# Optimization experiments

Measured on AMD Instinct MI355X. Metric: run time of the kernel, lower is better.

Reference implementation:

```python
import jax, jax.numpy as jnp
import numpy as np
import math

B, IN, H = 4096, 1024, 1024

def setup_inputs() -> dict:
    key = jax.random.key(0)
    ks = jax.random.split(key, 20)
    stdv = 1.0 / math.sqrt(H)
    def U(k, shape):
        return jax.random.uniform(k, shape, jnp.float32, -stdv, stdv)
    inp = {
        'input_': jax.random.normal(ks[0], (B, IN), jnp.float32),
        'prev_h': jax.random.normal(ks[1], (B, H), jnp.float32),
        'prev_c': jax.random.normal(ks[2], (B, H), jnp.float32),
    }
    names = ['ii', 'hi', 'if_', 'hf', 'ig', 'hg', 'io', 'ho']
    for n, kw, kb in zip(names, ks[3:11], ks[11:19]):
        in_dim = IN if n[0] == 'i' else H
        inp['W_' + n] = U(kw, (H, in_dim))  # torch Linear weight is (out, in)
        inp['b_' + n] = U(kb, (H,))
    return inp

def reference(input_, prev_h, prev_c,
              W_ii, b_ii, W_hi, b_hi, W_if_, b_if_, W_hf, b_hf,
              W_ig, b_ig, W_hg, b_hg, W_io, b_io, W_ho, b_ho):
    # Fuse the 8 small GEMMs into 2 batched GEMMs over stacked gate weights.
    Wx = jnp.concatenate([W_ii, W_if_, W_ig, W_io], axis=0)   # (4H, IN)
    Wh = jnp.concatenate([W_hi, W_hf, W_hg, W_ho], axis=0)    # (4H, H)
    bx = jnp.concatenate([b_ii, b_if_, b_ig, b_io], axis=0)   # (4H,)
    bh = jnp.concatenate([b_hi, b_hf, b_hg, b_ho], axis=0)
    gates = input_ @ Wx.T + prev_h @ Wh.T + bx + bh           # (B, 4H)
    i, f, g, o = jnp.split(gates, 4, axis=-1)
    i = jax.nn.sigmoid(i)
    f = jax.nn.sigmoid(f)
    g = jnp.tanh(g)
    o = jax.nn.sigmoid(o)
    c = f * prev_c + i * g
    h = o * jnp.tanh(c)
    return (h, c)
```

## Files before the change

### kernel.cpp

```cpp
#include <hip/hip_runtime.h>
#include <hip/hip_bf16.h>
#include <stdint.h>


typedef __attribute__((ext_vector_type(8))) short bf16x8;
typedef __attribute__((ext_vector_type(4))) float f32x4;
typedef __attribute__((ext_vector_type(8))) unsigned short u16x8;

__device__ __forceinline__ unsigned short f2bf(float f) {
  union { float f; uint32_t u; } v; v.f = f;
  uint32_t u = v.u;
  u += 0x7FFFu + ((u >> 16) & 1);
  return (unsigned short)(u >> 16);
}
__device__ __forceinline__ float fast_sigmoid(float x) { return 1.f / (1.f + __expf(-x)); }
__device__ __forceinline__ float fast_tanh(float x) { return 1.f - 2.f / (1.f + __expf(2.f * x)); }

__global__ __launch_bounds__(256) void pack_kernel(
    const float* __restrict__ x, const float* __restrict__ hprev,
    const float* __restrict__ W_ii, const float* __restrict__ W_if,
    const float* __restrict__ W_ig, const float* __restrict__ W_io,
    const float* __restrict__ W_hi, const float* __restrict__ W_hf,
    const float* __restrict__ W_hg, const float* __restrict__ W_ho,
    unsigned short* __restrict__ Ap, unsigned short* __restrict__ Wp) {
  const int bid = blockIdx.x;
  const int k = threadIdx.x << 3;
  const float* src;
  unsigned short* dst;
  if (bid < 4096) {
    const int b = bid;
    src = (k < 1024) ? (x + (size_t)b * 1024 + k) : (hprev + (size_t)b * 1024 + (k - 1024));
    dst = Ap + (size_t)b * 2048 + k;
  } else {
    const int rp = bid - 4096;
    const int g = (rp >> 4) & 3;
    const int u = ((rp >> 6) << 4) | (rp & 15);
    const float* wx = (g == 0) ? W_ii : (g == 1) ? W_if : (g == 2) ? W_ig : W_io;
    const float* wh = (g == 0) ? W_hi : (g == 1) ? W_hf : (g == 2) ? W_hg : W_ho;
    src = (k < 1024) ? (wx + (size_t)u * 1024 + k) : (wh + (size_t)u * 1024 + (k - 1024));
    dst = Wp + (size_t)rp * 2048 + k;
  }
  float4 v0 = *(const float4*)src;
  float4 v1 = *(const float4*)(src + 4);
  u16x8 o;
  o[0] = f2bf(v0.x); o[1] = f2bf(v0.y); o[2] = f2bf(v0.z); o[3] = f2bf(v0.w);
  o[4] = f2bf(v1.x); o[5] = f2bf(v1.y); o[6] = f2bf(v1.z); o[7] = f2bf(v1.w);
  *(u16x8*)dst = o;
}


#define GL16(g, l)                                                                   \
  __builtin_amdgcn_global_load_lds(                                                  \
      (const __attribute__((address_space(1))) unsigned int*)(g),                    \
      (__attribute__((address_space(3))) unsigned int*)(l), 16, 0, 0)

#define STAGE_A(BUF, H, KT)                                                          \
  { GL16(pA0 + (size_t)(H) * 524288 + (size_t)(KT) * 128,                            \
         lds + (BUF) * 32768 + (H) * 16384 + wvoff);                                 \
    GL16(pA1 + (size_t)(H) * 524288 + (size_t)(KT) * 128,                            \
         lds + (BUF) * 32768 + (H) * 16384 + 8192 + wvoff); }
#define STAGE_B(BUF, H, KT)                                                          \
  { GL16(pB0 + (size_t)(H) * 524288 + (size_t)(KT) * 128,                            \
         lds + 65536 + (BUF) * 32768 + (H) * 16384 + wvoff);                         \
    GL16(pB1 + (size_t)(H) * 524288 + (size_t)(KT) * 128,                            \
         lds + 65536 + (BUF) * 32768 + (H) * 16384 + 8192 + wvoff); }

#define DS_A(BUF, QQ)                                                                \
  { const char* Ab_ = lds + (BUF) * 32768 + tbA + (QQ) * 4096;                       \
    a00 = *(const bf16x8*)(Ab_ + off0);        a01 = *(const bf16x8*)(Ab_ + off1);   \
    a10 = *(const bf16x8*)(Ab_ + 2048 + off0); a11 = *(const bf16x8*)(Ab_ + 2048 + off1); }

#define DS_B(BUF)                                                                    \
  { const char* Bb_ = lds + 65536 + (BUF) * 32768 + tbB;                             \
    _Pragma("unroll")                                                                \
    for (int ni = 0; ni < 4; ++ni) {                                                 \
      breg[ni][0] = *(const bf16x8*)(Bb_ + ni * 2048 + off0);                        \
      breg[ni][1] = *(const bf16x8*)(Bb_ + ni * 2048 + off1);                        \
    } }

#define MFMA_CLUSTER(QQ)                                                             \
  { __builtin_amdgcn_s_setprio(1);                                                   \
    _Pragma("unroll")                                                                \
    for (int ni = 0; ni < 4; ++ni) {                                                 \
      acc[2*(QQ)][ni]   = __builtin_amdgcn_mfma_f32_16x16x32_bf16(a00, breg[ni][0], acc[2*(QQ)][ni], 0,0,0);   \
      acc[2*(QQ)][ni]   = __builtin_amdgcn_mfma_f32_16x16x32_bf16(a01, breg[ni][1], acc[2*(QQ)][ni], 0,0,0);   \
      acc[2*(QQ)+1][ni] = __builtin_amdgcn_mfma_f32_16x16x32_bf16(a10, breg[ni][0], acc[2*(QQ)+1][ni], 0,0,0); \
      acc[2*(QQ)+1][ni] = __builtin_amdgcn_mfma_f32_16x16x32_bf16(a11, breg[ni][1], acc[2*(QQ)+1][ni], 0,0,0); \
    }                                                                                \
    __builtin_amdgcn_s_setprio(0); }

#define BAR()      __builtin_amdgcn_s_barrier()
#define LGKM0()    asm volatile("s_waitcnt lgkmcnt(0)" ::: "memory")
#define LGKM8()    asm volatile("s_waitcnt lgkmcnt(8)" ::: "memory")
#define VMC4()     asm volatile("s_waitcnt vmcnt(4)" ::: "memory")

__global__ __launch_bounds__(512, 2) void lstm_gemm_kernel(
    const unsigned short* __restrict__ Ap, const unsigned short* __restrict__ Wp,
    const float* __restrict__ b_ii, const float* __restrict__ b_hi,
    const float* __restrict__ b_if, const float* __restrict__ b_hf,
    const float* __restrict__ b_ig, const float* __restrict__ b_hg,
    const float* __restrict__ b_io, const float* __restrict__ b_ho,
    const float* __restrict__ prev_c,
    float* __restrict__ out_h, float* __restrict__ out_c) {
  __shared__ char lds[131072];

  const int tid  = threadIdx.x;
  const int lane = tid & 63;
  const int wv   = tid >> 6;
  const int wm   = wv >> 2;
  const int wn   = wv & 3;

  const int bid = blockIdx.x;
  const int sid = (bid & 7) * 32 + (bid >> 3);
  const int bx  = sid & 15;
  const int by  = sid >> 4;

  const int r0  = tid >> 3;
  const int r1  = (tid + 512) >> 3;
  const int kb0 = (((tid & 7) ^ ((r0 >> 1) & 7)) << 4);
  const int kb1 = (((tid & 7) ^ ((r1 >> 1) & 7)) << 4);
  const char* ApC = (const char*)Ap;
  const char* BpC = (const char*)Wp;
  const char* pA0 = ApC + (size_t)(bx * 256 + r0) * 4096 + kb0;
  const char* pA1 = ApC + (size_t)(bx * 256 + r1) * 4096 + kb1;
  const char* pB0 = BpC + (size_t)(by * 256 + r0) * 4096 + kb0;
  const char* pB1 = BpC + (size_t)(by * 256 + r1) * 4096 + kb1;
  const int wvoff = wv * 1024;

  const int qe   = (lane >> 4) ^ ((lane >> 1) & 7);
  const int off0 = qe << 4;
  const int off1 = (qe ^ 4) << 4;
  const int tbA = (wm * 128 + (lane & 15)) * 128;
  const int tbB = (wn * 64 + (lane & 15)) * 128;

  f32x4 acc[8][4];
#pragma unroll
  for (int mi = 0; mi < 8; ++mi)
#pragma unroll
    for (int ni = 0; ni < 4; ++ni) acc[mi][ni] = (f32x4){0.f, 0.f, 0.f, 0.f};

  bf16x8 breg[4][2];
  bf16x8 a00, a01, a10, a11;

  STAGE_B(0, 0, 0); STAGE_B(0, 1, 0);
  STAGE_A(0, 0, 0); STAGE_A(0, 1, 0);
  STAGE_B(1, 0, 1); STAGE_B(1, 1, 1);
  VMC4();
  BAR();

  for (int i = 0; i < 16; ++i) {
    const int T  = i << 1;
    const int k1 = (T + 1) & 31;
    const int k2 = (T + 2) & 31;
    const int k3 = (T + 3) & 31;

    DS_B(0); DS_A(0, 0);
    STAGE_A(1, 0, k1);
    LGKM8();
    BAR(); LGKM0();
    MFMA_CLUSTER(0);
    BAR();
    DS_A(0, 1);
    STAGE_A(1, 1, k1);
    BAR(); LGKM0();
    MFMA_CLUSTER(1);
    BAR();
    DS_A(0, 2);
    STAGE_B(0, 0, k2);
    BAR(); LGKM0();
    MFMA_CLUSTER(2);
    BAR();
    DS_A(0, 3);
    STAGE_B(0, 1, k2);
    VMC4();
    BAR(); LGKM0();
    MFMA_CLUSTER(3);
    BAR();
    DS_B(1); DS_A(1, 0);
    STAGE_A(0, 0, k2);
    LGKM8();
    BAR(); LGKM0();
    MFMA_CLUSTER(0);
    BAR();
    DS_A(1, 1);
    STAGE_A(0, 1, k2);
    BAR(); LGKM0();
    MFMA_CLUSTER(1);
    BAR();
    DS_A(1, 2);
    STAGE_B(1, 0, k3);
    BAR(); LGKM0();
    MFMA_CLUSTER(2);
    BAR();
    DS_A(1, 3);
    STAGE_B(1, 1, k3);
    VMC4();
    BAR(); LGKM0();
    MFMA_CLUSTER(3);
    BAR();
  }

  const int u = ((by * 4 + wn) << 4) + (lane & 15);
  const float bsum0 = b_ii[u] + b_hi[u];
  const float bsum1 = b_if[u] + b_hf[u];
  const float bsum2 = b_ig[u] + b_hg[u];
  const float bsum3 = b_io[u] + b_ho[u];
  const int row0 = bx * 256 + wm * 128 + ((lane >> 4) << 2);

#pragma unroll
  for (int mi = 0; mi < 8; ++mi) {
#pragma unroll
    for (int rr = 0; rr < 4; ++rr) {
      const int row = row0 + mi * 16 + rr;
      const float gi = fast_sigmoid(acc[mi][0][rr] + bsum0);
      const float gf = fast_sigmoid(acc[mi][1][rr] + bsum1);
      const float gg = fast_tanh   (acc[mi][2][rr] + bsum2);
      const float go = fast_sigmoid(acc[mi][3][rr] + bsum3);
      const float cp = prev_c[(size_t)row * 1024 + u];
      const float c  = gf * cp + gi * gg;
      const float hh = go * fast_tanh(c);
      out_h[(size_t)row * 1024 + u] = hh;
      out_c[(size_t)row * 1024 + u] = c;
    }
  }
}


extern "C" void kernel_launch(void* const* d_in, const int* in_sizes, int n_in,
                              void* d_out, int out_size, void* d_ws, size_t ws_size,
                              hipStream_t stream) {
  const float* input_ = (const float*)d_in[0];
  const float* prev_h = (const float*)d_in[1];
  const float* prev_c = (const float*)d_in[2];
  const float* W_ii = (const float*)d_in[3];  const float* b_ii = (const float*)d_in[4];
  const float* W_hi = (const float*)d_in[5];  const float* b_hi = (const float*)d_in[6];
  const float* W_if = (const float*)d_in[7];  const float* b_if = (const float*)d_in[8];
  const float* W_hf = (const float*)d_in[9];  const float* b_hf = (const float*)d_in[10];
  const float* W_ig = (const float*)d_in[11]; const float* b_ig = (const float*)d_in[12];
  const float* W_hg = (const float*)d_in[13]; const float* b_hg = (const float*)d_in[14];
  const float* W_io = (const float*)d_in[15]; const float* b_io = (const float*)d_in[16];
  const float* W_ho = (const float*)d_in[17]; const float* b_ho = (const float*)d_in[18];

  unsigned short* Ap = (unsigned short*)d_ws;
  unsigned short* Wp = Ap + (size_t)4096 * 2048;

  pack_kernel<<<8192, 256, 0, stream>>>(input_, prev_h,
                                        W_ii, W_if, W_ig, W_io,
                                        W_hi, W_hf, W_hg, W_ho, Ap, Wp);

  float* out_h = (float*)d_out;
  float* out_c = out_h + (size_t)4096 * 1024;
  lstm_gemm_kernel<<<256, 512, 0, stream>>>(Ap, Wp,
                                            b_ii, b_hi, b_if, b_hf,
                                            b_ig, b_hg, b_io, b_ho,
                                            prev_c, out_h, out_c);
}
```

Before: 211.6 us.

## Double-buffer LDS fragment registers to overlap ds_reads with MFMA clusters

Splits the A and B register fragments into two ping-pong sets so the LDS reads for the next quarter-tile are issued before the MFMA cluster that consumes the current set. The explicit lgkmcnt waits are removed, which leaves the compiler to insert them. The aim is to hide LDS read latency behind matrix math instead of stalling before each cluster. In exchange it raises VGPR pressure under the 512-thread, 2-block launch bound, and the prefetch of the next B buffer happens later relative to its global staging, so correctness depends on the barrier placement.

```diff
diff --git a/kernel.cpp b/kernel.cpp
--- a/kernel.cpp
+++ b/kernel.cpp
@@ -65,33 +65,31 @@
     GL16(pB1 + (size_t)(H) * 524288 + (size_t)(KT) * 128,                            \
          lds + 65536 + (BUF) * 32768 + (H) * 16384 + 8192 + wvoff); }
 
-#define DS_A(BUF, QQ)                                                                \
+#define DS_A_INTO(A0f, A1f, A2f, A3f, BUF, QQ)                                       \
   { const char* Ab_ = lds + (BUF) * 32768 + tbA + (QQ) * 4096;                       \
-    a00 = *(const bf16x8*)(Ab_ + off0);        a01 = *(const bf16x8*)(Ab_ + off1);   \
-    a10 = *(const bf16x8*)(Ab_ + 2048 + off0); a11 = *(const bf16x8*)(Ab_ + 2048 + off1); }
-
-#define DS_B(BUF)                                                                    \
+    A0f = *(const bf16x8*)(Ab_ + off0);        A1f = *(const bf16x8*)(Ab_ + off1);   \
+    A2f = *(const bf16x8*)(Ab_ + 2048 + off0); A3f = *(const bf16x8*)(Ab_ + 2048 + off1); }
+
+#define DS_B_INTO(BR, BUF)                                                           \
   { const char* Bb_ = lds + 65536 + (BUF) * 32768 + tbB;                             \
     _Pragma("unroll")                                                                \
     for (int ni = 0; ni < 4; ++ni) {                                                 \
-      breg[ni][0] = *(const bf16x8*)(Bb_ + ni * 2048 + off0);                        \
-      breg[ni][1] = *(const bf16x8*)(Bb_ + ni * 2048 + off1);                        \
+      BR[ni][0] = *(const bf16x8*)(Bb_ + ni * 2048 + off0);                          \
+      BR[ni][1] = *(const bf16x8*)(Bb_ + ni * 2048 + off1);                          \
     } }
 
-#define MFMA_CLUSTER(QQ)                                                             \
+#define MFMA_C(QQ, A0f, A1f, A2f, A3f, BR)                                           \
   { __builtin_amdgcn_s_setprio(1);                                                   \
     _Pragma("unroll")                                                                \
     for (int ni = 0; ni < 4; ++ni) {                                                 \
-      acc[2*(QQ)][ni]   = __builtin_amdgcn_mfma_f32_16x16x32_bf16(a00, breg[ni][0], acc[2*(QQ)][ni], 0,0,0);   \
-      acc[2*(QQ)][ni]   = __builtin_amdgcn_mfma_f32_16x16x32_bf16(a01, breg[ni][1], acc[2*(QQ)][ni], 0,0,0);   \
-      acc[2*(QQ)+1][ni] = __builtin_amdgcn_mfma_f32_16x16x32_bf16(a10, breg[ni][0], acc[2*(QQ)+1][ni], 0,0,0); \
-      acc[2*(QQ)+1][ni] = __builtin_amdgcn_mfma_f32_16x16x32_bf16(a11, breg[ni][1], acc[2*(QQ)+1][ni], 0,0,0); \
+      acc[2*(QQ)][ni]   = __builtin_amdgcn_mfma_f32_16x16x32_bf16(A0f, BR[ni][0], acc[2*(QQ)][ni], 0,0,0);   \
+      acc[2*(QQ)][ni]   = __builtin_amdgcn_mfma_f32_16x16x32_bf16(A1f, BR[ni][1], acc[2*(QQ)][ni], 0,0,0);   \
+      acc[2*(QQ)+1][ni] = __builtin_amdgcn_mfma_f32_16x16x32_bf16(A2f, BR[ni][0], acc[2*(QQ)+1][ni], 0,0,0); \
+      acc[2*(QQ)+1][ni] = __builtin_amdgcn_mfma_f32_16x16x32_bf16(A3f, BR[ni][1], acc[2*(QQ)+1][ni], 0,0,0); \
     }                                                                                \
     __builtin_amdgcn_s_setprio(0); }
 
 #define BAR()      __builtin_amdgcn_s_barrier()
-#define LGKM0()    asm volatile("s_waitcnt lgkmcnt(0)" ::: "memory")
-#define LGKM8()    asm volatile("s_waitcnt lgkmcnt(8)" ::: "memory")
 #define VMC4()     asm volatile("s_waitcnt vmcnt(4)" ::: "memory")
 
 __global__ __launch_bounds__(512, 2) void lstm_gemm_kernel(
@@ -139,14 +137,16 @@
 #pragma unroll
     for (int ni = 0; ni < 4; ++ni) acc[mi][ni] = (f32x4){0.f, 0.f, 0.f, 0.f};
 
-  bf16x8 breg[4][2];
-  bf16x8 a00, a01, a10, a11;
+  bf16x8 bA[4][2], bB[4][2];
+  bf16x8 aX0, aX1, aX2, aX3, aY0, aY1, aY2, aY3;
 
   STAGE_B(0, 0, 0); STAGE_B(0, 1, 0);
   STAGE_A(0, 0, 0); STAGE_A(0, 1, 0);
   STAGE_B(1, 0, 1); STAGE_B(1, 1, 1);
   VMC4();
   BAR();
+  DS_B_INTO(bA, 0);
+  DS_A_INTO(aX0, aX1, aX2, aX3, 0, 0);
 
   for (int i = 0; i < 16; ++i) {
     const int T  = i << 1;
@@ -154,49 +154,49 @@
     const int k2 = (T + 2) & 31;
     const int k3 = (T + 3) & 31;
 
-    DS_B(0); DS_A(0, 0);
     STAGE_A(1, 0, k1);
-    LGKM8();
-    BAR(); LGKM0();
-    MFMA_CLUSTER(0);
-    BAR();
-    DS_A(0, 1);
+    BAR();
+    DS_A_INTO(aY0, aY1, aY2, aY3, 0, 1);
+    MFMA_C(0, aX0, aX1, aX2, aX3, bA);
+    BAR();
     STAGE_A(1, 1, k1);
-    BAR(); LGKM0();
-    MFMA_CLUSTER(1);
-    BAR();
-    DS_A(0, 2);
+    BAR();
+    DS_A_INTO(aX0, aX1, aX2, aX3, 0, 2);
+    MFMA_C(1, aY0, aY1, aY2, aY3, bA);
+    BAR();
     STAGE_B(0, 0, k2);
-    BAR(); LGKM0();
-    MFMA_CLUSTER(2);
-    BAR();
-    DS_A(0, 3);
+    BAR();
+    DS_A_INTO(aY0, aY1, aY2, aY3, 0, 3);
+    MFMA_C(2, aX0, aX1, aX2, aX3, bA);
+    BAR();
     STAGE_B(0, 1, k2);
     VMC4();
-    BAR(); LGKM0();
-    MFMA_CLUSTER(3);
-    BAR();
-    DS_B(1); DS_A(1, 0);
+    BAR();
+    DS_B_INTO(bB, 1);
+    DS_A_INTO(aX0, aX1, aX2, aX3, 1, 0);
+    MFMA_C(3, aY0, aY1, aY2, aY3, bA);
+    BAR();
     STAGE_A(0, 0, k2);
-    LGKM8();
-    BAR(); LGKM0();
-    MFMA_CLUSTER(0);
-    BAR();
-    DS_A(1, 1);
+    BAR();
+    DS_A_INTO(aY0, aY1, aY2, aY3, 1, 1);
+    MFMA_C(0, aX0, aX1, aX2, aX3, bB);
+    BAR();
     STAGE_A(0, 1, k2);
-    BAR(); LGKM0();
-    MFMA_CLUSTER(1);
-    BAR();
-    DS_A(1, 2);
+    BAR();
+    DS_A_INTO(aX0, aX1, aX2, aX3, 1, 2);
+    MFMA_C(1, aY0, aY1, aY2, aY3, bB);
+    BAR();
     STAGE_B(1, 0, k3);
-    BAR(); LGKM0();
-    MFMA_CLUSTER(2);
-    BAR();
-    DS_A(1, 3);
+    BAR();
+    DS_A_INTO(aY0, aY1, aY2, aY3, 1, 3);
+    MFMA_C(2, aX0, aX1, aX2, aX3, bB);
+    BAR();
     STAGE_B(1, 1, k3);
     VMC4();
-    BAR(); LGKM0();
-    MFMA_CLUSTER(3);
+    BAR();
+    DS_B_INTO(bA, 0);
+    DS_A_INTO(aX0, aX1, aX2, aX3, 0, 0);
+    MFMA_C(3, aY0, aY1, aY2, aY3, bB);
     BAR();
   }
 
```

After: 209.6 us. Within noise of the previous version (-0.9%).
